# Kernel optimization log

Measured on AMD Instinct MI355X. Metric: run time of the kernel, lower is better.

## Reference

```python
import jax, jax.numpy as jnp
import numpy as np

B, V, E, N = 4, 16384, 4, 32
F, U = 1024, 1024


def setup_inputs() -> dict:
    key = jax.random.key(0)
    k1, k2, k3 = jax.random.split(key, 3)
    # adjacency values in [-1, V); -1 marks non-existent neighbours
    adjacency = jax.random.randint(k1, (B, V, E, N), -1, V, dtype=jnp.int32)
    # force some vertices to be fully invalid (all -1) so the mask path matters
    invalid_vertex = jax.random.uniform(k2, (B, V, 1, 1)) < 0.25
    adjacency = jnp.where(invalid_vertex, jnp.int32(-1), adjacency)
    features = jax.random.normal(k3, (B, V, F), dtype=jnp.float32)
    kernel = jax.random.normal(jax.random.fold_in(key, 10), (F, U), dtype=jnp.float32) * (1.0 / np.sqrt(F))
    bias = jnp.zeros((U,), dtype=jnp.float32)
    return {"adjacency": adjacency, "features": features, "kernel": kernel, "bias": bias}


def reference(adjacency, features, kernel, bias):
    # A vertex is "valid" if it has at least one neighbour (any adjacency entry >= 0)
    valid = jnp.any(adjacency >= 0, axis=(2, 3))  # [B, V]
    # Dense per-node linear transform (1x1-conv analogue) + bias + relu
    out = jax.nn.relu(jnp.einsum('bvf,fu->bvu', features, kernel) + bias)  # [B, V, U]
    f_in, f_out = kernel.shape
    if f_in == f_out:
        def_features = features  # invalid vertices keep their input features
    else:
        def_features = jnp.zeros(features.shape[:-1] + (f_out,), dtype=features.dtype)
    # scatter transformed features back only at valid vertices
    return jnp.where(valid[..., None], out, def_features)
```

## Files before the change

kernel.cpp:

```cpp
#include <hip/hip_runtime.h>

#define MTOT 65536
#define KTOT 1024
#define NTOT 1024

#define BM 256
#define BN 256
#define BK 32
#define NSTEP (KTOT / BK)
#define NCHUNK 4096

typedef __attribute__((ext_vector_type(4))) unsigned int u32x4;
typedef __attribute__((ext_vector_type(4))) float f32x4;
typedef __attribute__((ext_vector_type(8))) __bf16 bf16x8;
typedef __attribute__((ext_vector_type(4))) unsigned short u16x4;

static __device__ __forceinline__ unsigned short f2bf(float f) {
    unsigned int u = __float_as_uint(f);
    u += 0x7fffu + ((u >> 16) & 1u);
    return (unsigned short)(u >> 16);
}

#define GLOAD16(g, l)                                                              \
    __builtin_amdgcn_global_load_lds(                                              \
        (const __attribute__((address_space(1))) void*)(g),                        \
        (__attribute__((address_space(3))) void*)(l), 16, 0, 0)

#define VMCNT(n) asm volatile("s_waitcnt vmcnt(" #n ")" ::: "memory")
#define CFENCE   asm volatile("" ::: "memory")
#define BAR()    __builtin_amdgcn_s_barrier()

__global__ __launch_bounds__(256) void valid_count_kernel(const int* __restrict__ adj,
                                                          unsigned char* __restrict__ valid,
                                                          int* __restrict__ chunkcnt) {
    __shared__ int vb[16];
    const int c    = blockIdx.x;
    const int tid  = threadIdx.x;
    const int wv   = tid >> 6;
    const int lane = tid & 63;
#pragma unroll
    for (int r = 0; r < 4; ++r) {
        const int row = c * 16 + wv * 4 + r;
        const int2 a2 = reinterpret_cast<const int2*>(adj)[(size_t)row * 64 + lane];
        const int anyv = __any((a2.x >= 0) || (a2.y >= 0));
        if (lane == 0) { vb[wv * 4 + r] = anyv; valid[row] = (unsigned char)anyv; }
    }
    __syncthreads();
    if (tid == 0) {
        int s = 0;
#pragma unroll
        for (int i = 0; i < 16; ++i) s += vb[i];
        chunkcnt[c] = s;
    }
}

__global__ __launch_bounds__(1024) void scan_kernel(const int* __restrict__ chunkcnt,
                                                    int* __restrict__ chunkoff,
                                                    int* __restrict__ nv) {
    __shared__ int sc[1024];
    const int t = threadIdx.x;
    const int b = t * 4;
    const int c0 = chunkcnt[b], c1 = chunkcnt[b + 1], c2 = chunkcnt[b + 2], c3 = chunkcnt[b + 3];
    const int s = c0 + c1 + c2 + c3;
    sc[t] = s;
    __syncthreads();
    for (int d = 1; d < 1024; d <<= 1) {
        const int v = (t >= d) ? sc[t - d] : 0;
        __syncthreads();
        sc[t] += v;
        __syncthreads();
    }
    const int excl = sc[t] - s;
    chunkoff[b]     = excl;
    chunkoff[b + 1] = excl + c0;
    chunkoff[b + 2] = excl + c0 + c1;
    chunkoff[b + 3] = excl + c0 + c1 + c2;
    if (t == 1023) nv[0] = sc[t];
}

__global__ __launch_bounds__(256) void prep_compact_kernel(const unsigned char* __restrict__ valid,
                                                           const int* __restrict__ chunkoff,
                                                           const float* __restrict__ feat,
                                                           unsigned short* __restrict__ abf,
                                                           int* __restrict__ cidx,
                                                           float* __restrict__ out) {
    __shared__ int cposL[16];
    __shared__ int vL[16];
    const int c    = blockIdx.x;
    const int tid  = threadIdx.x;
    const int wv   = tid >> 6;
    const int lane = tid & 63;

    if (tid < 64) {
        const int v = (lane < 16) ? (int)valid[c * 16 + lane] : 0;
        const unsigned long long mask = __ballot(v != 0);
        if (lane < 16) {
            const int pc = __popcll(mask & ((1ull << lane) - 1ull));
            const int cp = chunkoff[c] + pc;
            cposL[lane] = cp;
            vL[lane]    = v;
            if (v) cidx[cp] = c * 16 + lane;
        }
    }
    __syncthreads();

#pragma unroll
    for (int r = 0; r < 4; ++r) {
        const int li  = wv * 4 + r;
        const int row = c * 16 + li;
        const f32x4* frow = reinterpret_cast<const f32x4*>(feat + (size_t)row * KTOT);
        if (vL[li]) {
            u16x4* brow = reinterpret_cast<u16x4*>(abf + (size_t)cposL[li] * KTOT);
#pragma unroll
            for (int i = 0; i < 4; ++i) {
                const f32x4 v = frow[lane + 64 * i];
                u16x4 b;
                b.x = f2bf(v[0]); b.y = f2bf(v[1]); b.z = f2bf(v[2]); b.w = f2bf(v[3]);
                brow[lane + 64 * i] = b;
            }
        } else {
            f32x4* orow = reinterpret_cast<f32x4*>(out + (size_t)row * NTOT);
#pragma unroll
            for (int i = 0; i < 4; ++i)
                orow[lane + 64 * i] = frow[lane + 64 * i];
        }
    }
}

__global__ __launch_bounds__(256) void transposeB_kernel(const float* __restrict__ kern,
                                                         unsigned short* __restrict__ kT) {
    __shared__ float tile[32][33];
    const int bx = blockIdx.x & 31;
    const int by = blockIdx.x >> 5;
    const int tx = threadIdx.x & 31;
    const int ty = threadIdx.x >> 5;
#pragma unroll
    for (int r = 0; r < 4; ++r)
        tile[ty + r * 8][tx] = kern[(size_t)(by * 32 + ty + r * 8) * NTOT + bx * 32 + tx];
    __syncthreads();
#pragma unroll
    for (int r = 0; r < 4; ++r)
        kT[(size_t)(bx * 32 + ty + r * 8) * KTOT + by * 32 + tx] = f2bf(tile[tx][ty + r * 8]);
}

__global__ __launch_bounds__(1024, 4) void gemm_kernel(const unsigned short* __restrict__ A,
                                                       const unsigned short* __restrict__ Bt,
                                                       const float* __restrict__ bias,
                                                       const int* __restrict__ cidx,
                                                       const int* __restrict__ nv,
                                                       float* __restrict__ out) {
    __shared__ __align__(16) unsigned short Asm[4 * 8192];
    __shared__ __align__(16) unsigned short Bsm[4 * 8192];

    const int nvalid = nv[0];

    const int tid  = threadIdx.x;
    const int lane = tid & 63;
    const int wv   = tid >> 6;
    const int wm   = wv >> 2;
    const int wn   = wv & 3;

    const int xcd = (int)blockIdx.x & 7;
    const int idx = (int)blockIdx.x >> 3;
    const int bm  = (idx >> 2) * 8 + xcd;
    const int bn  = idx & 3;
    const int m0i = bm * BM;
    if (m0i >= nvalid) return;
    const size_t m0 = (size_t)m0i;
    const int    n0 = bn * BN;

    const int srow   = tid >> 2;
    const int lch    = (tid & 3) ^ ((tid >> 3) & 3);
    const size_t s_goff = (size_t)srow * KTOT + lch * 8;
    const int    s_loff = wv << 9;

    const unsigned short* Agl = A  + m0 * (size_t)KTOT + s_goff;
    const unsigned short* Bgl = Bt + (size_t)n0 * KTOT + s_goff;

#define STAGE(b, kt) do {                                                          \
        GLOAD16(Agl + (kt) * BK, &Asm[(b) * 8192 + s_loff]);                       \
        GLOAD16(Bgl + (kt) * BK, &Bsm[(b) * 8192 + s_loff]);                       \
    } while (0)

    const int lr  = lane & 15;
    const int g4  = lane >> 4;
    const int rsw = (g4 ^ ((lr >> 1) & 3)) << 3;
    int aridx[4], bridx[4];
#pragma unroll
    for (int m = 0; m < 4; ++m)
        aridx[m] = (wm * 64 + m * 16 + lr) * BK + rsw;
#pragma unroll
    for (int n = 0; n < 4; ++n)
        bridx[n] = (wn * 64 + n * 16 + lr) * BK + rsw;

    f32x4 acc[4][4];
#pragma unroll
    for (int m = 0; m < 4; ++m)
#pragma unroll
        for (int n = 0; n < 4; ++n)
            acc[m][n] = {0.0f, 0.0f, 0.0f, 0.0f};

    STAGE(0, 0);
    STAGE(1, 1);
    STAGE(2, 2);
    VMCNT(4);
    BAR(); CFENCE;

#pragma unroll
    for (int t = 0; t < NSTEP; ++t) {
        if (t + 3 < NSTEP) STAGE((t + 3) & 3, t + 3);
        const int b = t & 3;
        bf16x8 af[4], bfr[4];
#pragma unroll
        for (int n = 0; n < 4; ++n)
            bfr[n] = __builtin_bit_cast(bf16x8, *reinterpret_cast<const u32x4*>(&Bsm[b * 8192 + bridx[n]]));
#pragma unroll
        for (int m = 0; m < 4; ++m)
            af[m] = __builtin_bit_cast(bf16x8, *reinterpret_cast<const u32x4*>(&Asm[b * 8192 + aridx[m]]));
        __builtin_amdgcn_s_setprio(1);
#pragma unroll
        for (int m = 0; m < 4; ++m)
#pragma unroll
            for (int n = 0; n < 4; ++n)
                acc[m][n] = __builtin_amdgcn_mfma_f32_16x16x32_bf16(af[m], bfr[n], acc[m][n], 0, 0, 0);
        __builtin_amdgcn_s_setprio(0);
        if (t < NSTEP - 3)       VMCNT(4);
        else if (t == NSTEP - 3) VMCNT(2);
        else if (t == NSTEP - 2) VMCNT(0);
        if (t < NSTEP - 1) { BAR(); CFENCE; }
    }

    float bv[4];
#pragma unroll
    for (int n = 0; n < 4; ++n)
        bv[n] = bias[n0 + wn * 64 + n * 16 + lr];

#pragma unroll
    for (int m = 0; m < 4; ++m) {
#pragma unroll
        for (int q = 0; q < 4; ++q) {
            const int cr = m0i + wm * 64 + m * 16 + g4 * 4 + q;
            if (cr < nvalid) {
                const int orow = cidx[cr];
                const size_t ro = (size_t)orow * NTOT + n0 + wn * 64 + lr;
#pragma unroll
                for (int n = 0; n < 4; ++n)
                    out[ro + n * 16] = fmaxf(acc[m][n][q] + bv[n], 0.0f);
            }
        }
    }
#undef STAGE
}

__global__ __launch_bounds__(256) void prep_full_kernel(const int* __restrict__ adj,
                                                        const float* __restrict__ feat,
                                                        unsigned short* __restrict__ abf,
                                                        unsigned char* __restrict__ valid,
                                                        float* __restrict__ out) {
    const int row  = blockIdx.x * 4 + (threadIdx.x >> 6);
    const int lane = threadIdx.x & 63;
    const int2 a2  = reinterpret_cast<const int2*>(adj)[(size_t)row * 64 + lane];
    const bool anyv = __any((a2.x >= 0) || (a2.y >= 0)) != 0;
    const f32x4* frow = reinterpret_cast<const f32x4*>(feat + (size_t)row * KTOT);
    u16x4*       brow = reinterpret_cast<u16x4*>(abf + (size_t)row * KTOT);
    f32x4*       orow = reinterpret_cast<f32x4*>(out + (size_t)row * NTOT);
    if (anyv) {
#pragma unroll
        for (int i = 0; i < 4; ++i) {
            const f32x4 v = frow[lane + 64 * i];
            u16x4 b;
            b.x = f2bf(v[0]); b.y = f2bf(v[1]); b.z = f2bf(v[2]); b.w = f2bf(v[3]);
            brow[lane + 64 * i] = b;
        }
    } else {
#pragma unroll
        for (int i = 0; i < 4; ++i)
            orow[lane + 64 * i] = frow[lane + 64 * i];
    }
    if (lane == 0) valid[row] = anyv ? 1 : 0;
}

__global__ __launch_bounds__(1024, 4) void gemm_full_kernel(const unsigned short* __restrict__ A,
                                                            const unsigned short* __restrict__ Bt,
                                                            const float* __restrict__ bias,
                                                            const unsigned char* __restrict__ valid,
                                                            float* __restrict__ out) {
    __shared__ __align__(16) unsigned short Asm[4 * 8192];
    __shared__ __align__(16) unsigned short Bsm[4 * 8192];
    const int tid  = threadIdx.x;
    const int lane = tid & 63;
    const int wv   = tid >> 6;
    const int wm   = wv >> 2;
    const int wn   = wv & 3;
    const int cpx = (int)gridDim.x >> 3;
    const int swz = ((int)blockIdx.x & 7) * cpx + ((int)blockIdx.x >> 3);
    const int bm  = swz >> 2;
    const int bn  = swz & 3;
    const size_t m0 = (size_t)bm * BM;
    const int    n0 = bn * BN;
    const int srow   = tid >> 2;
    const int lch    = (tid & 3) ^ ((tid >> 3) & 3);
    const size_t s_goff = (size_t)srow * KTOT + lch * 8;
    const int    s_loff = wv << 9;
    const unsigned short* Agl = A  + m0 * (size_t)KTOT + s_goff;
    const unsigned short* Bgl = Bt + (size_t)n0 * KTOT + s_goff;
#define STAGE(b, kt) do {                                                          \
        GLOAD16(Agl + (kt) * BK, &Asm[(b) * 8192 + s_loff]);                       \
        GLOAD16(Bgl + (kt) * BK, &Bsm[(b) * 8192 + s_loff]);                       \
    } while (0)
    const int lr  = lane & 15;
    const int g4  = lane >> 4;
    const int rsw = (g4 ^ ((lr >> 1) & 3)) << 3;
    int aridx[4], bridx[4];
#pragma unroll
    for (int m = 0; m < 4; ++m) aridx[m] = (wm * 64 + m * 16 + lr) * BK + rsw;
#pragma unroll
    for (int n = 0; n < 4; ++n) bridx[n] = (wn * 64 + n * 16 + lr) * BK + rsw;
    f32x4 acc[4][4];
#pragma unroll
    for (int m = 0; m < 4; ++m)
#pragma unroll
        for (int n = 0; n < 4; ++n) acc[m][n] = {0.f, 0.f, 0.f, 0.f};
    STAGE(0, 0); STAGE(1, 1); STAGE(2, 2);
    VMCNT(4); BAR(); CFENCE;
#pragma unroll
    for (int t = 0; t < NSTEP; ++t) {
        if (t + 3 < NSTEP) STAGE((t + 3) & 3, t + 3);
        const int b = t & 3;
        bf16x8 af[4], bfr[4];
#pragma unroll
        for (int n = 0; n < 4; ++n)
            bfr[n] = __builtin_bit_cast(bf16x8, *reinterpret_cast<const u32x4*>(&Bsm[b * 8192 + bridx[n]]));
#pragma unroll
        for (int m = 0; m < 4; ++m)
            af[m] = __builtin_bit_cast(bf16x8, *reinterpret_cast<const u32x4*>(&Asm[b * 8192 + aridx[m]]));
#pragma unroll
        for (int m = 0; m < 4; ++m)
#pragma unroll
            for (int n = 0; n < 4; ++n)
                acc[m][n] = __builtin_amdgcn_mfma_f32_16x16x32_bf16(af[m], bfr[n], acc[m][n], 0, 0, 0);
        if (t < NSTEP - 3)       VMCNT(4);
        else if (t == NSTEP - 3) VMCNT(2);
        else if (t == NSTEP - 2) VMCNT(0);
        if (t < NSTEP - 1) { BAR(); CFENCE; }
    }
    float bv[4];
#pragma unroll
    for (int n = 0; n < 4; ++n) bv[n] = bias[n0 + wn * 64 + n * 16 + lr];
#pragma unroll
    for (int m = 0; m < 4; ++m) {
#pragma unroll
        for (int q = 0; q < 4; ++q) {
            const size_t row = m0 + wm * 64 + m * 16 + g4 * 4 + q;
            if (valid[row]) {
                const size_t ro = row * NTOT + n0 + wn * 64 + lr;
#pragma unroll
                for (int n = 0; n < 4; ++n)
                    out[ro + n * 16] = fmaxf(acc[m][n][q] + bv[n], 0.0f);
            }
        }
    }
#undef STAGE
}

extern "C" void kernel_launch(void* const* d_in, const int* in_sizes, int n_in,
                              void* d_out, int out_size, void* d_ws, size_t ws_size,
                              hipStream_t stream) {
    const int*   adj  = (const int*)d_in[0];
    const float* feat = (const float*)d_in[1];
    const float* kern = (const float*)d_in[2];
    const float* bias = (const float*)d_in[3];
    float* out = (float*)d_out;

    char* ws = (char*)d_ws;
    unsigned short* kT    = (unsigned short*)ws;
    unsigned char*  valid = (unsigned char*)(ws + (2u << 20));
    int*  cidx     = (int*)(ws + (2u << 20) + (64u << 10));
    int*  chunkcnt = (int*)(ws + (2u << 20) + (320u << 10));
    int*  chunkoff = (int*)(ws + (2u << 20) + (336u << 10));
    int*  nv       = (int*)(ws + (2u << 20) + (352u << 10));
    unsigned short* abf = (unsigned short*)(ws + (4u << 20));

    const size_t need = (4ull << 20) + (size_t)MTOT * KTOT * 2;

    transposeB_kernel<<<(KTOT / 32) * (NTOT / 32), 256, 0, stream>>>(kern, kT);
    if (ws_size >= need) {
        valid_count_kernel<<<NCHUNK, 256, 0, stream>>>(adj, valid, chunkcnt);
        scan_kernel<<<1, 1024, 0, stream>>>(chunkcnt, chunkoff, nv);
        prep_compact_kernel<<<NCHUNK, 256, 0, stream>>>(valid, chunkoff, feat, abf, cidx, out);
        gemm_kernel<<<(MTOT / BM) * (NTOT / BN), 1024, 0, stream>>>(abf, kT, bias, cidx, nv, out);
    } else {
        unsigned short* abf_fb = (unsigned short*)(ws + (2u << 20) + (64u << 10));
        prep_full_kernel<<<MTOT / 4, 256, 0, stream>>>(adj, feat, abf_fb, valid, out);
        gemm_full_kernel<<<(MTOT / BM) * (NTOT / BN), 1024, 0, stream>>>(abf_fb, kT, bias, valid, out);
    }
}
```

Measured before the change: 240.9 us.

## Fuse validity check and compaction into one kernel using atomic counter

Replaces the three-stage validity count, global prefix scan, and compaction pipeline with a single kernel. Each block computes its own validity mask and reserves output slots with an atomicAdd on a global counter. This removes two kernel launches and the serial scan, but compacted row order becomes nondeterministic. It also adds a memset before the fused kernel.

Result: slower. 260.3 us (+8.0%).

```diff
diff --git a/kernel.cpp b/kernel.cpp
--- a/kernel.cpp
+++ b/kernel.cpp
@@ -30,75 +30,40 @@
 #define CFENCE   asm volatile("" ::: "memory")
 #define BAR()    __builtin_amdgcn_s_barrier()
 
-__global__ __launch_bounds__(256) void valid_count_kernel(const int* __restrict__ adj,
-                                                          unsigned char* __restrict__ valid,
-                                                          int* __restrict__ chunkcnt) {
-    __shared__ int vb[16];
+__global__ __launch_bounds__(256) void prep_fused_kernel(const int* __restrict__ adj,
+                                                         const float* __restrict__ feat,
+                                                         unsigned short* __restrict__ abf,
+                                                         int* __restrict__ cidx,
+                                                         float* __restrict__ out,
+                                                         int* __restrict__ counter) {
+    __shared__ int vL[16];
+    __shared__ int cposL[16];
     const int c    = blockIdx.x;
     const int tid  = threadIdx.x;
     const int wv   = tid >> 6;
     const int lane = tid & 63;
+
 #pragma unroll
     for (int r = 0; r < 4; ++r) {
-        const int row = c * 16 + wv * 4 + r;
+        const int li  = wv * 4 + r;
+        const int row = c * 16 + li;
         const int2 a2 = reinterpret_cast<const int2*>(adj)[(size_t)row * 64 + lane];
         const int anyv = __any((a2.x >= 0) || (a2.y >= 0));
-        if (lane == 0) { vb[wv * 4 + r] = anyv; valid[row] = (unsigned char)anyv; }
+        if (lane == 0) vL[li] = anyv;
     }
     __syncthreads();
-    if (tid == 0) {
-        int s = 0;
-#pragma unroll
-        for (int i = 0; i < 16; ++i) s += vb[i];
-        chunkcnt[c] = s;
-    }
-}
-
-__global__ __launch_bounds__(1024) void scan_kernel(const int* __restrict__ chunkcnt,
-                                                    int* __restrict__ chunkoff,
-                                                    int* __restrict__ nv) {
-    __shared__ int sc[1024];
-    const int t = threadIdx.x;
-    const int b = t * 4;
-    const int c0 = chunkcnt[b], c1 = chunkcnt[b + 1], c2 = chunkcnt[b + 2], c3 = chunkcnt[b + 3];
-    const int s = c0 + c1 + c2 + c3;
-    sc[t] = s;
-    __syncthreads();
-    for (int d = 1; d < 1024; d <<= 1) {
-        const int v = (t >= d) ? sc[t - d] : 0;
-        __syncthreads();
-        sc[t] += v;
-        __syncthreads();
-    }
-    const int excl = sc[t] - s;
-    chunkoff[b]     = excl;
-    chunkoff[b + 1] = excl + c0;
-    chunkoff[b + 2] = excl + c0 + c1;
-    chunkoff[b + 3] = excl + c0 + c1 + c2;
-    if (t == 1023) nv[0] = sc[t];
-}
-
-__global__ __launch_bounds__(256) void prep_compact_kernel(const unsigned char* __restrict__ valid,
-                                                           const int* __restrict__ chunkoff,
-                                                           const float* __restrict__ feat,
-                                                           unsigned short* __restrict__ abf,
-                                                           int* __restrict__ cidx,
-                                                           float* __restrict__ out) {
-    __shared__ int cposL[16];
-    __shared__ int vL[16];
-    const int c    = blockIdx.x;
-    const int tid  = threadIdx.x;
-    const int wv   = tid >> 6;
-    const int lane = tid & 63;
 
     if (tid < 64) {
-        const int v = (lane < 16) ? (int)valid[c * 16 + lane] : 0;
+        const int v = (lane < 16) ? vL[lane] : 0;
         const unsigned long long mask = __ballot(v != 0);
+        const int cnt = __popcll(mask);
+        int base = 0;
+        if (lane == 0 && cnt) base = atomicAdd(counter, cnt);
+        base = __shfl(base, 0);
         if (lane < 16) {
             const int pc = __popcll(mask & ((1ull << lane) - 1ull));
-            const int cp = chunkoff[c] + pc;
+            const int cp = base + pc;
             cposL[lane] = cp;
-            vL[lane]    = v;
             if (v) cidx[cp] = c * 16 + lane;
         }
     }
@@ -375,19 +340,16 @@
     char* ws = (char*)d_ws;
     unsigned short* kT    = (unsigned short*)ws;
     unsigned char*  valid = (unsigned char*)(ws + (2u << 20));
-    int*  cidx     = (int*)(ws + (2u << 20) + (64u << 10));
-    int*  chunkcnt = (int*)(ws + (2u << 20) + (320u << 10));
-    int*  chunkoff = (int*)(ws + (2u << 20) + (336u << 10));
-    int*  nv       = (int*)(ws + (2u << 20) + (352u << 10));
+    int*  cidx = (int*)(ws + (2u << 20) + (64u << 10));
+    int*  nv   = (int*)(ws + (2u << 20) + (352u << 10));
     unsigned short* abf = (unsigned short*)(ws + (4u << 20));
 
     const size_t need = (4ull << 20) + (size_t)MTOT * KTOT * 2;
 
     transposeB_kernel<<<(KTOT / 32) * (NTOT / 32), 256, 0, stream>>>(kern, kT);
     if (ws_size >= need) {
-        valid_count_kernel<<<NCHUNK, 256, 0, stream>>>(adj, valid, chunkcnt);
-        scan_kernel<<<1, 1024, 0, stream>>>(chunkcnt, chunkoff, nv);
-        prep_compact_kernel<<<NCHUNK, 256, 0, stream>>>(valid, chunkoff, feat, abf, cidx, out);
+        hipMemsetAsync(nv, 0, sizeof(int), stream);
+        prep_fused_kernel<<<NCHUNK, 256, 0, stream>>>(adj, feat, abf, cidx, out, nv);
         gemm_kernel<<<(MTOT / BM) * (NTOT / BN), 1024, 0, stream>>>(abf, kT, bias, cidx, nv, out);
     } else {
         unsigned short* abf_fb = (unsigned short*)(ws + (2u << 20) + (64u << 10));
```
